# Performance work log

Hardware: AMD Instinct MI355X
Metric: run time of the kernel (lower is better)

The kernel has to match this reference:

```python
import jax, jax.numpy as jnp
import numpy as np

B, S, D = 2, 2048, 2048
H = 16
HD = D // H            # 128 head dim
L = 512                # latent dim
R = 64                 # rope dim (min(64, HD) = 64)
RH = R // 2
SCALE = HD ** -0.5     # note: uses head_dim, not head_dim+rope_dim
NEG = jnp.float32(-1e9)


def _rope_tables():
    inv_freq = 1.0 / (10000.0 ** (jnp.arange(0, R, 2, dtype=jnp.float32) / R))  # [RH]
    pos = jnp.arange(S, dtype=jnp.float32)
    freqs = pos[:, None] * inv_freq[None, :]  # [S, RH]
    return jnp.cos(freqs), jnp.sin(freqs)


def _apply_rope(x, cos, sin):
    # x: [B, H, S, R], interleaved even/odd rotation as in the torch source
    xe, xo = x[..., 0::2], x[..., 1::2]                    # [B,H,S,RH]
    c = cos[None, None]
    s = sin[None, None]
    re = xe * c - xo * s
    ro = xe * s + xo * c
    return jnp.stack([re, ro], axis=-1).reshape(x.shape)   # re-interleave


def setup_inputs() -> dict:
    key = jax.random.key(0)
    ks = jax.random.split(key, 8)
    std = 0.02
    f32 = jnp.float32
    return {
        "x":     jax.random.normal(ks[0], (B, S, D), f32),
        "W_ckv": jax.random.normal(ks[1], (D, L), f32) * std,      # compress_kv
        "W_kv":  jax.random.normal(ks[2], (L, 2 * D), f32) * std,  # kv_proj
        "W_cq":  jax.random.normal(ks[3], (D, L), f32) * std,      # compress_q
        "W_q":   jax.random.normal(ks[4], (L, D), f32) * std,      # q_proj
        "W_qr":  jax.random.normal(ks[5], (L, H * R), f32) * std,  # q_rope
        "W_kr":  jax.random.normal(ks[6], (L, R), f32) * std,      # k_rope
        "W_out": jax.random.normal(ks[7], (D, D), f32) * std,      # out_proj
    }


def reference(x, W_ckv, W_kv, W_cq, W_q, W_qr, W_kr, W_out):
    cos, sin = _rope_tables()

    c_kv = x @ W_ckv                                   # [B,S,L]
    kv = c_kv @ W_kv                                   # [B,S,2D]
    c_q = x @ W_cq                                     # [B,S,L]

    q_c = (c_q @ W_q).reshape(B, S, H, HD).transpose(0, 2, 1, 3)    # [B,H,S,HD]
    q_r = (c_q @ W_qr).reshape(B, S, H, R).transpose(0, 2, 1, 3)    # [B,H,S,R]
    k_r = (c_kv @ W_kr)[:, None, :, :]                               # [B,1,S,R]

    k_c, v = jnp.split(kv, 2, axis=-1)
    k_c = k_c.reshape(B, S, H, HD).transpose(0, 2, 1, 3)             # [B,H,S,HD]
    v = v.reshape(B, S, H, HD).transpose(0, 2, 1, 3)                 # [B,H,S,HD]

    q_r = _apply_rope(q_r, cos, sin)
    k_r = jnp.broadcast_to(_apply_rope(k_r, cos, sin), (B, H, S, R))

    q = jnp.concatenate([q_c, q_r], axis=-1)                         # [B,H,S,HD+R]
    k = jnp.concatenate([k_c, k_r], axis=-1)                         # [B,H,S,HD+R]

    scores = jnp.einsum("bhqd,bhkd->bhqk", q, k) * SCALE             # [B,H,S,S]
    causal = jnp.tril(jnp.ones((S, S), dtype=bool))
    scores = jnp.where(causal[None, None], scores, NEG)
    p = jax.nn.softmax(scores, axis=-1)
    attended = jnp.einsum("bhqk,bhkd->bhqd", p, v)                   # [B,H,S,HD]

    out = attended.transpose(0, 2, 1, 3).reshape(B, S, D) @ W_out    # [B,S,D]
    return out  # dropout is identity in eval / p=0
```

## Files before the change

### kernel.cpp

```cpp
#include <hip/hip_runtime.h>
#include <hip/hip_bf16.h>
#include <cstdint>
#include <cstddef>

typedef __bf16 bf16;
typedef __attribute__((ext_vector_type(2))) __bf16 bf16x2;
typedef __attribute__((ext_vector_type(4))) __bf16 bf16x4;
typedef __attribute__((ext_vector_type(8))) __bf16 bf16x8;
typedef __attribute__((ext_vector_type(4))) float f32x4;

#define MFMA16(a, b, c) __builtin_amdgcn_mfma_f32_16x16x32_bf16((a), (b), (c), 0, 0, 0)
#define SCALE_L2E 0.127517432f

#define QCR_STRIDE 3072
#define KV_STRIDE  4160

__device__ __forceinline__ void gload16(const void* g, void* l) {
    __builtin_amdgcn_global_load_lds(
        (const __attribute__((address_space(1))) void*)g,
        (__attribute__((address_space(3))) void*)l, 16, 0, 0);
}

__device__ __forceinline__ void bar_lgkm() {
    asm volatile("s_waitcnt lgkmcnt(0)" ::: "memory");
    __builtin_amdgcn_s_barrier();
    asm volatile("" ::: "memory");
}

__global__ void k_cvt(const float* __restrict__ in, bf16* __restrict__ out, int n4)
{
    int i = blockIdx.x * blockDim.x + threadIdx.x;
    int stride = gridDim.x * blockDim.x;
    const float4* in4 = (const float4*)in;
    bf16x4* o4 = (bf16x4*)out;
    for (; i < n4; i += stride) {
        float4 v = in4[i];
        bf16x4 o;
        o[0] = (bf16)v.x; o[1] = (bf16)v.y; o[2] = (bf16)v.z; o[3] = (bf16)v.w;
        o4[i] = o;
    }
}

__global__ __launch_bounds__(256) void k_cvtT(const float* __restrict__ in,
                                              bf16* __restrict__ out, int Kd, int Nd)
{
    __shared__ float tile[32][33];
    const int k0 = blockIdx.y * 32, n0 = blockIdx.x * 32;
    const int t = threadIdx.x;
    const int r = t >> 3, c4 = (t & 7) * 4;
    float4 v = *(const float4*)(in + (size_t)(k0 + r) * Nd + n0 + c4);
    tile[r][c4 + 0] = v.x; tile[r][c4 + 1] = v.y;
    tile[r][c4 + 2] = v.z; tile[r][c4 + 3] = v.w;
    __syncthreads();
    bf16x4 o;
    o[0] = (bf16)tile[c4 + 0][r]; o[1] = (bf16)tile[c4 + 1][r];
    o[2] = (bf16)tile[c4 + 2][r]; o[3] = (bf16)tile[c4 + 3][r];
    *(bf16x4*)(out + (size_t)(n0 + r) * Kd + k0 + c4) = o;
}

template<int NF, bool F32OUT>
__global__ __launch_bounds__(256) void k_gemm_bt(
    const bf16* __restrict__ A, const bf16* __restrict__ BT,
    bf16* __restrict__ Cb, float* __restrict__ Cf,
    int M, int N, int K, int lda)
{
    __shared__ bf16 As[2][4096];
    __shared__ bf16 Bs[2][NF * 1024];

    const int t = threadIdx.x;
    const int m0 = blockIdx.y * 128;
    const int n0 = blockIdx.x * (NF * 32);
    const int wid = t >> 6, lane = t & 63;
    const int wm = (wid >> 1) * 64, wn = (wid & 1) * (NF * 16);
    const int lr = lane & 15, lk = (lane >> 4) * 8;

    const int srow = t >> 2, skc = (t & 3) << 3;
    const int bn0 = min(n0 + srow, N - 1);
    const int bn1 = min(n0 + srow + 64, N - 1);

    f32x4 acc[4][NF];
    const f32x4 z = {0.f, 0.f, 0.f, 0.f};
#pragma unroll
    for (int m = 0; m < 4; ++m)
#pragma unroll
        for (int n = 0; n < NF; ++n) acc[m][n] = z;

    auto stage = [&](int buf, int k0) {
        gload16(BT + (size_t)bn0 * K + k0 + skc, &Bs[buf][t * 8]);
        if constexpr (NF == 4)
            gload16(BT + (size_t)bn1 * K + k0 + skc, &Bs[buf][(t + 256) * 8]);
        gload16(A + (size_t)(m0 + srow) * lda + k0 + skc, &As[buf][t * 8]);
        gload16(A + (size_t)(m0 + srow + 64) * lda + k0 + skc, &As[buf][(t + 256) * 8]);
    };

    stage(0, 0);
    __syncthreads();

    for (int k0 = 0; k0 < K; k0 += 32) {
        const int cur = (k0 >> 5) & 1;
        if (k0 + 32 < K) stage(cur ^ 1, k0 + 32);

        bf16x8 af[4], bfr[NF];
#pragma unroll
        for (int m = 0; m < 4; ++m) af[m] = *(const bf16x8*)(&As[cur][(wm + m * 16 + lr) * 32 + lk]);
#pragma unroll
        for (int n = 0; n < NF; ++n) bfr[n] = *(const bf16x8*)(&Bs[cur][(wn + n * 16 + lr) * 32 + lk]);
#pragma unroll
        for (int m = 0; m < 4; ++m)
#pragma unroll
            for (int n = 0; n < NF; ++n)
                acc[m][n] = MFMA16(af[m], bfr[n], acc[m][n]);

        __syncthreads();
    }

    const int lrow4 = (lane >> 4) * 4;
#pragma unroll
    for (int m = 0; m < 4; ++m)
#pragma unroll
        for (int n = 0; n < NF; ++n)
#pragma unroll
            for (int i = 0; i < 4; ++i) {
                int r = m0 + wm + m * 16 + lrow4 + i;
                int c = n0 + wn + n * 16 + lr;
                if (r < M && c < N) {
                    if constexpr (F32OUT) Cf[(size_t)r * N + c] = acc[m][n][i];
                    else Cb[(size_t)r * N + c] = (bf16)acc[m][n][i];
                }
            }
}

__global__ void k_rope_q(bf16* __restrict__ qcr)
{
    int idx = blockIdx.x * blockDim.x + threadIdx.x;
    int row = idx >> 9;
    int rem = idx & 511;
    int h = rem >> 5;
    int i = rem & 31;
    int s = row & 2047;
    float ang = (float)s * __expf(-(float)i * 0.28782313662f);
    float c = cosf(ang), sn = sinf(ang);
    size_t base = (size_t)row * QCR_STRIDE + 2048 + h * 64 + (i << 1);
    float xe = (float)qcr[base], xo = (float)qcr[base + 1];
    qcr[base] = (bf16)(xe * c - xo * sn);
    qcr[base + 1] = (bf16)(xe * sn + xo * c);
}

__global__ void k_rope_k(bf16* __restrict__ kvkr)
{
    int idx = blockIdx.x * blockDim.x + threadIdx.x;
    int row = idx >> 5;
    int i = idx & 31;
    int s = row & 2047;
    float ang = (float)s * __expf(-(float)i * 0.28782313662f);
    float c = cosf(ang), sn = sinf(ang);
    size_t base = (size_t)row * KV_STRIDE + 4096 + (i << 1);
    float xe = (float)kvkr[base], xo = (float)kvkr[base + 1];
    kvkr[base] = (bf16)(xe * c - xo * sn);
    kvkr[base + 1] = (bf16)(xe * sn + xo * c);
}

__global__ __launch_bounds__(512, 2) void k_attn(
    const bf16* __restrict__ qcr, const bf16* __restrict__ kvkr,
    bf16* __restrict__ att)
{
    __shared__ bf16 Ks[128 * 200];
    __shared__ bf16 Vt[128 * 136];
    __shared__ bf16 Pw[8][16 * 136];

    const int L = blockIdx.x;
    const int p = L >> 5;
    const int bh = L & 31;
    const int h = bh & 15, b = bh >> 4;

    const int t = threadIdx.x;
    const int wid = t >> 6, lane = t & 63;
    const int lr = lane & 15, lk = (lane >> 4) * 8, lrow4 = (lane >> 4) * 4;
    const size_t rowbase = (size_t)b * 2048;

    const int kcrow = t >> 4, kcfc = (t & 15) << 3;
    const int krrow = t >> 3, krfc = (t & 7) << 3;
    const int vk = (t & 63) * 2;
    const int vf = (t >> 6) * 8;

    const f32x4 z = {0.f, 0.f, 0.f, 0.f};

    bf16x8 rc[4], rr[2], rv[4];
    auto LOAD = [&](int kb) {
#pragma unroll
        for (int i = 0; i < 4; ++i)
            rc[i] = *(const bf16x8*)(kvkr + (rowbase + kb + kcrow + 32 * i) * KV_STRIDE + h * 128 + kcfc);
#pragma unroll
        for (int i = 0; i < 2; ++i)
            rr[i] = *(const bf16x8*)(kvkr + (rowbase + kb + krrow + 64 * i) * KV_STRIDE + 4096 + krfc);
#pragma unroll
        for (int i = 0; i < 2; ++i) {
            const bf16* vs = kvkr + (rowbase + kb + vk) * KV_STRIDE + 2048 + h * 128 + vf + 64 * i;
            rv[2 * i]     = *(const bf16x8*)vs;
            rv[2 * i + 1] = *(const bf16x8*)(vs + KV_STRIDE);
        }
    };
    auto WRITE = [&]() {
#pragma unroll
        for (int i = 0; i < 4; ++i)
            *(bf16x8*)(Ks + (kcrow + 32 * i) * 200 + kcfc) = rc[i];
#pragma unroll
        for (int i = 0; i < 2; ++i)
            *(bf16x8*)(Ks + (krrow + 64 * i) * 200 + 128 + krfc) = rr[i];
#pragma unroll
        for (int i = 0; i < 2; ++i)
#pragma unroll
            for (int j = 0; j < 8; ++j) {
                bf16x2 pr; pr[0] = rv[2 * i][j]; pr[1] = rv[2 * i + 1][j];
                *(bf16x2*)(Vt + (vf + 64 * i + j) * 136 + vk) = pr;
            }
    };

    LOAD(0);

#pragma unroll 1
    for (int pass = 0; pass < 2; ++pass) {
        const int qt = pass ? 15 - p : p;
        const int qrow_w = qt * 128 + wid * 16;

        bf16x8 qf[6];
        {
            const size_t qrow = rowbase + qrow_w + lr;
            const bf16* qp = qcr + qrow * QCR_STRIDE + h * 128;
#pragma unroll
            for (int ks = 0; ks < 4; ++ks) qf[ks] = *(const bf16x8*)(qp + ks * 32 + lk);
            const bf16* qp2 = qcr + qrow * QCR_STRIDE + 2048 + h * 64;
#pragma unroll
            for (int ks = 0; ks < 2; ++ks) qf[4 + ks] = *(const bf16x8*)(qp2 + ks * 32 + lk);
        }

        float mrow[4], lsum[4];
        f32x4 o[8];
#pragma unroll
        for (int i = 0; i < 4; ++i) { mrow[i] = -3e38f; lsum[i] = 0.f; }
#pragma unroll
        for (int n = 0; n < 8; ++n) o[n] = z;

        const int nkt = qt + 1;
#pragma unroll 1
        for (int kt = 0; kt < nkt; ++kt) {
            const int kb = kt * 128;
            bar_lgkm();
            WRITE();
            if (kt + 1 < nkt) LOAD(kb + 128);
            else if (pass == 0) LOAD(0);
            bar_lgkm();

            f32x4 sacc[8];
#pragma unroll
            for (int kg = 0; kg < 8; ++kg) {
                f32x4 s = z;
#pragma unroll
                for (int ks = 0; ks < 6; ++ks) {
                    bf16x8 kf = *(const bf16x8*)(Ks + (kg * 16 + lr) * 200 + ks * 32 + lk);
                    s = MFMA16(qf[ks], kf, s);
                }
                sacc[kg] = s;
            }

            const bool domask = (kb + 127) > qrow_w;
            float rmax[4];
#pragma unroll
            for (int i = 0; i < 4; ++i) {
                int qi = qrow_w + lrow4 + i;
                float mx = -3e38f;
#pragma unroll
                for (int kg = 0; kg < 8; ++kg) {
                    float v = sacc[kg][i] * SCALE_L2E;
                    if (domask && (kb + kg * 16 + lr) > qi) v = -3e38f;
                    sacc[kg][i] = v;
                    mx = fmaxf(mx, v);
                }
                rmax[i] = mx;
            }
#pragma unroll
            for (int d = 1; d < 16; d <<= 1)
#pragma unroll
                for (int i = 0; i < 4; ++i)
                    rmax[i] = fmaxf(rmax[i], __shfl_xor(rmax[i], d, 64));

            int anynew = 0;
#pragma unroll
            for (int i = 0; i < 4; ++i)
                if (rmax[i] > mrow[i]) anynew = 1;
            if (__any(anynew)) {
#pragma unroll
                for (int i = 0; i < 4; ++i) {
                    float mnew = fmaxf(mrow[i], rmax[i]);
                    float scl = __builtin_amdgcn_exp2f(mrow[i] - mnew);
                    mrow[i] = mnew;
                    lsum[i] *= scl;
#pragma unroll
                    for (int n = 0; n < 8; ++n) o[n][i] *= scl;
                }
            }

            float rsum[4] = {0.f, 0.f, 0.f, 0.f};
#pragma unroll
            for (int kg = 0; kg < 8; ++kg)
#pragma unroll
                for (int i = 0; i < 4; ++i) {
                    float pv = __builtin_amdgcn_exp2f(sacc[kg][i] - mrow[i]);
                    sacc[kg][i] = pv;
                    rsum[i] += pv;
                }
#pragma unroll
            for (int d = 1; d < 16; d <<= 1)
#pragma unroll
                for (int i = 0; i < 4; ++i) rsum[i] += __shfl_xor(rsum[i], d, 64);
#pragma unroll
            for (int i = 0; i < 4; ++i) lsum[i] += rsum[i];

#pragma unroll
            for (int kg = 0; kg < 8; ++kg)
#pragma unroll
                for (int i = 0; i < 4; ++i)
                    Pw[wid][(lrow4 + i) * 136 + kg * 16 + lr] = (bf16)sacc[kg][i];

#pragma unroll
            for (int ks = 0; ks < 4; ++ks) {
                bf16x8 pa = *(const bf16x8*)(&Pw[wid][lr * 136 + ks * 32 + lk]);
#pragma unroll
                for (int n = 0; n < 8; ++n) {
                    bf16x8 vfr = *(const bf16x8*)(Vt + (n * 16 + lr) * 136 + ks * 32 + lk);
                    o[n] = MFMA16(pa, vfr, o[n]);
                }
            }
        }

#pragma unroll
        for (int i = 0; i < 4; ++i) {
            float inv = 1.f / lsum[i];
            size_t orow = (rowbase + qrow_w + lrow4 + i) * 2048 + h * 128;
#pragma unroll
            for (int n = 0; n < 8; ++n)
                att[orow + n * 16 + lr] = (bf16)(o[n][i] * inv);
        }
    }
}

extern "C" void kernel_launch(void* const* d_in, const int* in_sizes, int n_in,
                              void* d_out, int out_size, void* d_ws, size_t ws_size,
                              hipStream_t stream)
{
    (void)in_sizes; (void)n_in; (void)out_size; (void)ws_size;
    const float* x = (const float*)d_in[0];
    const float* w_ckv = (const float*)d_in[1];
    const float* w_kv = (const float*)d_in[2];
    const float* w_cq = (const float*)d_in[3];
    const float* w_q = (const float*)d_in[4];
    const float* w_qr = (const float*)d_in[5];
    const float* w_kr = (const float*)d_in[6];
    const float* w_out = (const float*)d_in[7];
    float* out = (float*)d_out;

    char* ws = (char*)d_ws;
    size_t off = 0;
    auto take = [&](size_t elems) -> bf16* {
        bf16* p = (bf16*)(ws + off);
        off += (elems * sizeof(bf16) + 255) & ~(size_t)255;
        return p;
    };
    bf16* WCT    = take(1024ull * 2048);
    bf16* WKVKRT = take(4160ull * 512);
    bf16* WQQRT  = take(3072ull * 512);
    bf16* C      = take(4096ull * 1024);
    bf16* KVKR   = take(4096ull * 4160);
    bf16* QCR    = take(4096ull * 3072);
    bf16* ATT    = take(4096ull * 2048);
    bf16* WOUTT  = C;
    bf16* XB     = KVKR;

    auto cvtT = [&](const float* in, bf16* o, int K, int N) {
        k_cvtT<<<dim3(N / 32, K / 32), 256, 0, stream>>>(in, o, K, N);
    };
    cvtT(w_ckv, WCT, 2048, 512);
    cvtT(w_cq, WCT + 512ull * 2048, 2048, 512);
    cvtT(w_kv, WKVKRT, 512, 4096);
    cvtT(w_kr, WKVKRT + 4096ull * 512, 512, 64);
    cvtT(w_q, WQQRT, 512, 2048);
    cvtT(w_qr, WQQRT + 2048ull * 512, 512, 1024);

    k_cvt<<<2048, 256, 0, stream>>>(x, XB, (4096 * 2048) / 4);

    k_gemm_bt<2, false><<<dim3(16, 32), 256, 0, stream>>>(
        XB, WCT, C, nullptr, 4096, 1024, 2048, 2048);
    k_gemm_bt<4, false><<<dim3(33, 32), 256, 0, stream>>>(
        C, WKVKRT, KVKR, nullptr, 4096, 4160, 512, 1024);
    k_gemm_bt<4, false><<<dim3(24, 32), 256, 0, stream>>>(
        C + 512, WQQRT, QCR, nullptr, 4096, 3072, 512, 1024);

    cvtT(w_out, WOUTT, 2048, 2048);

    k_rope_q<<<8192, 256, 0, stream>>>(QCR);
    k_rope_k<<<512, 256, 0, stream>>>(KVKR);

    k_attn<<<256, 512, 0, stream>>>(QCR, KVKR, ATT);

    k_gemm_bt<4, true><<<dim3(16, 32), 256, 0, stream>>>(
        ATT, WOUTT, nullptr, out, 4096, 2048, 2048, 2048);
}
```

Measured before the change: 292.4 us.

## Split attention into one q-tile per block with 64-key tiles and folded scale

The attention kernel changes from 256 blocks that each process two paired q-tiles to 512 blocks with one q-tile each. Key tiles shrink from 128 to 64, which cuts LDS use so four blocks can be resident per CU. Warps skip key tiles that lie fully above their causal rows. The softmax scale times log2(e) is folded into the Q projection GEMM epilogue, and the row sums are taken with an extra MFMA against a ones vector instead of shuffle reductions. The cost is twice as many loop iterations and barriers per key, and the load balance now depends on block scheduling rather than explicit pairing.

```diff
diff --git a/kernel.cpp b/kernel.cpp
--- a/kernel.cpp
+++ b/kernel.cpp
@@ -62,7 +62,7 @@
 __global__ __launch_bounds__(256) void k_gemm_bt(
     const bf16* __restrict__ A, const bf16* __restrict__ BT,
     bf16* __restrict__ Cb, float* __restrict__ Cf,
-    int M, int N, int K, int lda)
+    int M, int N, int K, int lda, float cscale)
 {
     __shared__ bf16 As[2][4096];
     __shared__ bf16 Bs[2][NF * 1024];
@@ -124,8 +124,9 @@
                 int r = m0 + wm + m * 16 + lrow4 + i;
                 int c = n0 + wn + n * 16 + lr;
                 if (r < M && c < N) {
-                    if constexpr (F32OUT) Cf[(size_t)r * N + c] = acc[m][n][i];
-                    else Cb[(size_t)r * N + c] = (bf16)acc[m][n][i];
+                    float val = acc[m][n][i] * cscale;
+                    if constexpr (F32OUT) Cf[(size_t)r * N + c] = val;
+                    else Cb[(size_t)r * N + c] = (bf16)val;
                 }
             }
 }
@@ -160,17 +161,19 @@
     kvkr[base + 1] = (bf16)(xe * sn + xo * c);
 }
 
-__global__ __launch_bounds__(512, 2) void k_attn(
+__global__ __launch_bounds__(512, 4) void k_attn(
     const bf16* __restrict__ qcr, const bf16* __restrict__ kvkr,
     bf16* __restrict__ att)
 {
-    __shared__ bf16 Ks[128 * 200];
-    __shared__ bf16 Vt[128 * 136];
-    __shared__ bf16 Pw[8][16 * 136];
+    __shared__ bf16 Ks[64 * 200];
+    __shared__ bf16 Vt[128 * 72];
+    __shared__ bf16 Pw[8][16 * 72];
 
     const int L = blockIdx.x;
-    const int p = L >> 5;
-    const int bh = L & 31;
+    const int base = L & 255;
+    const int bh = base & 31;
+    const int qtg = base >> 5;
+    const int qt = (L < 256) ? qtg : 15 - qtg;
     const int h = bh & 15, b = bh >> 4;
 
     const int t = threadIdx.x;
@@ -180,167 +183,151 @@
 
     const int kcrow = t >> 4, kcfc = (t & 15) << 3;
     const int krrow = t >> 3, krfc = (t & 7) << 3;
-    const int vk = (t & 63) * 2;
-    const int vf = (t >> 6) * 8;
+    const int vk = (t & 31) * 2;
+    const int vf = (t >> 5) * 8;
 
     const f32x4 z = {0.f, 0.f, 0.f, 0.f};
 
-    bf16x8 rc[4], rr[2], rv[4];
+    bf16x8 rc0, rc1, rr, rv0, rv1;
     auto LOAD = [&](int kb) {
+        rc0 = *(const bf16x8*)(kvkr + (rowbase + kb + kcrow) * KV_STRIDE + h * 128 + kcfc);
+        rc1 = *(const bf16x8*)(kvkr + (rowbase + kb + kcrow + 32) * KV_STRIDE + h * 128 + kcfc);
+        rr  = *(const bf16x8*)(kvkr + (rowbase + kb + krrow) * KV_STRIDE + 4096 + krfc);
+        const bf16* vs = kvkr + (rowbase + kb + vk) * KV_STRIDE + 2048 + h * 128 + vf;
+        rv0 = *(const bf16x8*)vs;
+        rv1 = *(const bf16x8*)(vs + KV_STRIDE);
+    };
+    auto WRITE = [&]() {
+        *(bf16x8*)(Ks + kcrow * 200 + kcfc) = rc0;
+        *(bf16x8*)(Ks + (kcrow + 32) * 200 + kcfc) = rc1;
+        *(bf16x8*)(Ks + krrow * 200 + 128 + krfc) = rr;
+#pragma unroll
+        for (int j = 0; j < 8; ++j) {
+            bf16x2 pr; pr[0] = rv0[j]; pr[1] = rv1[j];
+            *(bf16x2*)(Vt + (vf + j) * 72 + vk) = pr;
+        }
+    };
+
+    const int qrow_w = qt * 128 + wid * 16;
+
+    bf16x8 qf[6];
+    {
+        const size_t qrow = rowbase + qrow_w + lr;
+        const bf16* qp = qcr + qrow * QCR_STRIDE + h * 128;
+#pragma unroll
+        for (int ks = 0; ks < 4; ++ks) qf[ks] = *(const bf16x8*)(qp + ks * 32 + lk);
+        const bf16* qp2 = qcr + qrow * QCR_STRIDE + 2048 + h * 64;
+#pragma unroll
+        for (int ks = 0; ks < 2; ++ks) qf[4 + ks] = *(const bf16x8*)(qp2 + ks * 32 + lk);
+    }
+
+    bf16x8 ones;
+#pragma unroll
+    for (int j = 0; j < 8; ++j) ones[j] = (bf16)1.0f;
+
+    float mrow[4], lsum[4];
+    f32x4 o[8];
+#pragma unroll
+    for (int i = 0; i < 4; ++i) { mrow[i] = -3e38f; lsum[i] = 0.f; }
+#pragma unroll
+    for (int n = 0; n < 8; ++n) o[n] = z;
+
+    const int nkt = 2 * qt + 2;
+    LOAD(0);
+
+#pragma unroll 1
+    for (int kt = 0; kt < nkt; ++kt) {
+        const int kb = kt * 64;
+        bar_lgkm();
+        WRITE();
+        if (kt + 1 < nkt) LOAD(kb + 64);
+        bar_lgkm();
+
+        if (kb > qrow_w + 15) continue;
+
+        f32x4 sacc[4];
+#pragma unroll
+        for (int kg = 0; kg < 4; ++kg) {
+            f32x4 s = z;
+#pragma unroll
+            for (int ks = 0; ks < 6; ++ks) {
+                bf16x8 kf = *(const bf16x8*)(Ks + (kg * 16 + lr) * 200 + ks * 32 + lk);
+                s = MFMA16(qf[ks], kf, s);
+            }
+            sacc[kg] = s;
+        }
+
+        const bool domask = (kb + 63) > qrow_w;
+        float rmax[4];
+#pragma unroll
+        for (int i = 0; i < 4; ++i) {
+            int qi = qrow_w + lrow4 + i;
+            float mx = -3e38f;
+#pragma unroll
+            for (int kg = 0; kg < 4; ++kg) {
+                float v = sacc[kg][i];
+                if (domask && (kb + kg * 16 + lr) > qi) v = -3e38f;
+                sacc[kg][i] = v;
+                mx = fmaxf(mx, v);
+            }
+            rmax[i] = mx;
+        }
+#pragma unroll
+        for (int d = 1; d < 16; d <<= 1)
+#pragma unroll
+            for (int i = 0; i < 4; ++i)
+                rmax[i] = fmaxf(rmax[i], __shfl_xor(rmax[i], d, 64));
+
+        int anynew = 0;
 #pragma unroll
         for (int i = 0; i < 4; ++i)
-            rc[i] = *(const bf16x8*)(kvkr + (rowbase + kb + kcrow + 32 * i) * KV_STRIDE + h * 128 + kcfc);
-#pragma unroll
-        for (int i = 0; i < 2; ++i)
-            rr[i] = *(const bf16x8*)(kvkr + (rowbase + kb + krrow + 64 * i) * KV_STRIDE + 4096 + krfc);
-#pragma unroll
-        for (int i = 0; i < 2; ++i) {
-            const bf16* vs = kvkr + (rowbase + kb + vk) * KV_STRIDE + 2048 + h * 128 + vf + 64 * i;
-            rv[2 * i]     = *(const bf16x8*)vs;
-            rv[2 * i + 1] = *(const bf16x8*)(vs + KV_STRIDE);
-        }
-    };
-    auto WRITE = [&]() {
-#pragma unroll
-        for (int i = 0; i < 4; ++i)
-            *(bf16x8*)(Ks + (kcrow + 32 * i) * 200 + kcfc) = rc[i];
-#pragma unroll
-        for (int i = 0; i < 2; ++i)
-            *(bf16x8*)(Ks + (krrow + 64 * i) * 200 + 128 + krfc) = rr[i];
-#pragma unroll
-        for (int i = 0; i < 2; ++i)
-#pragma unroll
-            for (int j = 0; j < 8; ++j) {
-                bf16x2 pr; pr[0] = rv[2 * i][j]; pr[1] = rv[2 * i + 1][j];
-                *(bf16x2*)(Vt + (vf + 64 * i + j) * 136 + vk) = pr;
-            }
-    };
-
-    LOAD(0);
-
-#pragma unroll 1
-    for (int pass = 0; pass < 2; ++pass) {
-        const int qt = pass ? 15 - p : p;
-        const int qrow_w = qt * 128 + wid * 16;
-
-        bf16x8 qf[6];
-        {
-            const size_t qrow = rowbase + qrow_w + lr;
-            const bf16* qp = qcr + qrow * QCR_STRIDE + h * 128;
-#pragma unroll
-            for (int ks = 0; ks < 4; ++ks) qf[ks] = *(const bf16x8*)(qp + ks * 32 + lk);
-            const bf16* qp2 = qcr + qrow * QCR_STRIDE + 2048 + h * 64;
-#pragma unroll
-            for (int ks = 0; ks < 2; ++ks) qf[4 + ks] = *(const bf16x8*)(qp2 + ks * 32 + lk);
-        }
-
-        float mrow[4], lsum[4];
-        f32x4 o[8];
-#pragma unroll
-        for (int i = 0; i < 4; ++i) { mrow[i] = -3e38f; lsum[i] = 0.f; }
-#pragma unroll
-        for (int n = 0; n < 8; ++n) o[n] = z;
-
-        const int nkt = qt + 1;
-#pragma unroll 1
-        for (int kt = 0; kt < nkt; ++kt) {
-            const int kb = kt * 128;
-            bar_lgkm();
-            WRITE();
-            if (kt + 1 < nkt) LOAD(kb + 128);
-            else if (pass == 0) LOAD(0);
-            bar_lgkm();
-
-            f32x4 sacc[8];
-#pragma unroll
-            for (int kg = 0; kg < 8; ++kg) {
-                f32x4 s = z;
-#pragma unroll
-                for (int ks = 0; ks < 6; ++ks) {
-                    bf16x8 kf = *(const bf16x8*)(Ks + (kg * 16 + lr) * 200 + ks * 32 + lk);
-                    s = MFMA16(qf[ks], kf, s);
-                }
-                sacc[kg] = s;
-            }
-
-            const bool domask = (kb + 127) > qrow_w;
-            float rmax[4];
+            if (rmax[i] > mrow[i]) anynew = 1;
+        if (__any(anynew)) {
 #pragma unroll
             for (int i = 0; i < 4; ++i) {
-                int qi = qrow_w + lrow4 + i;
-                float mx = -3e38f;
-#pragma unroll
-                for (int kg = 0; kg < 8; ++kg) {
-                    float v = sacc[kg][i] * SCALE_L2E;
-                    if (domask && (kb + kg * 16 + lr) > qi) v = -3e38f;
-                    sacc[kg][i] = v;
-                    mx = fmaxf(mx, v);
-                }
-                rmax[i] = mx;
-            }
-#pragma unroll
-            for (int d = 1; d < 16; d <<= 1)
-#pragma unroll
-                for (int i = 0; i < 4; ++i)
-                    rmax[i] = fmaxf(rmax[i], __shfl_xor(rmax[i], d, 64));
-
-            int anynew = 0;
+                float mnew = fmaxf(mrow[i], rmax[i]);
+                float scl = __builtin_amdgcn_exp2f(mrow[i] - mnew);
+                mrow[i] = mnew;
+                lsum[i] *= scl;
+#pragma unroll
+                for (int n = 0; n < 8; ++n) o[n][i] *= scl;
+            }
+        }
+
+#pragma unroll
+        for (int kg = 0; kg < 4; ++kg)
 #pragma unroll
             for (int i = 0; i < 4; ++i)
-                if (rmax[i] > mrow[i]) anynew = 1;
-            if (__any(anynew)) {
-#pragma unroll
-                for (int i = 0; i < 4; ++i) {
-                    float mnew = fmaxf(mrow[i], rmax[i]);
-                    float scl = __builtin_amdgcn_exp2f(mrow[i] - mnew);
-                    mrow[i] = mnew;
-                    lsum[i] *= scl;
-#pragma unroll
-                    for (int n = 0; n < 8; ++n) o[n][i] *= scl;
-                }
-            }
-
-            float rsum[4] = {0.f, 0.f, 0.f, 0.f};
-#pragma unroll
-            for (int kg = 0; kg < 8; ++kg)
-#pragma unroll
-                for (int i = 0; i < 4; ++i) {
-                    float pv = __builtin_amdgcn_exp2f(sacc[kg][i] - mrow[i]);
-                    sacc[kg][i] = pv;
-                    rsum[i] += pv;
-                }
-#pragma unroll
-            for (int d = 1; d < 16; d <<= 1)
-#pragma unroll
-                for (int i = 0; i < 4; ++i) rsum[i] += __shfl_xor(rsum[i], d, 64);
-#pragma unroll
-            for (int i = 0; i < 4; ++i) lsum[i] += rsum[i];
-
-#pragma unroll
-            for (int kg = 0; kg < 8; ++kg)
-#pragma unroll
-                for (int i = 0; i < 4; ++i)
-                    Pw[wid][(lrow4 + i) * 136 + kg * 16 + lr] = (bf16)sacc[kg][i];
-
-#pragma unroll
-            for (int ks = 0; ks < 4; ++ks) {
-                bf16x8 pa = *(const bf16x8*)(&Pw[wid][lr * 136 + ks * 32 + lk]);
-#pragma unroll
-                for (int n = 0; n < 8; ++n) {
-                    bf16x8 vfr = *(const bf16x8*)(Vt + (n * 16 + lr) * 136 + ks * 32 + lk);
-                    o[n] = MFMA16(pa, vfr, o[n]);
-                }
-            }
-        }
-
-#pragma unroll
-        for (int i = 0; i < 4; ++i) {
-            float inv = 1.f / lsum[i];
-            size_t orow = (rowbase + qrow_w + lrow4 + i) * 2048 + h * 128;
-#pragma unroll
-            for (int n = 0; n < 8; ++n)
-                att[orow + n * 16 + lr] = (bf16)(o[n][i] * inv);
-        }
+                sacc[kg][i] = __builtin_amdgcn_exp2f(sacc[kg][i] - mrow[i]);
+
+#pragma unroll
+        for (int kg = 0; kg < 4; ++kg)
+#pragma unroll
+            for (int i = 0; i < 4; ++i)
+                Pw[wid][(lrow4 + i) * 72 + kg * 16 + lr] = (bf16)sacc[kg][i];
+
+        f32x4 rs = z;
+#pragma unroll
+        for (int ks = 0; ks < 2; ++ks) {
+            bf16x8 pa = *(const bf16x8*)(&Pw[wid][lr * 72 + ks * 32 + lk]);
+            rs = MFMA16(pa, ones, rs);
+#pragma unroll
+            for (int n = 0; n < 8; ++n) {
+                bf16x8 vfr = *(const bf16x8*)(Vt + (n * 16 + lr) * 72 + ks * 32 + lk);
+                o[n] = MFMA16(pa, vfr, o[n]);
+            }
+        }
+#pragma unroll
+        for (int i = 0; i < 4; ++i) lsum[i] += rs[i];
+    }
+
+#pragma unroll
+    for (int i = 0; i < 4; ++i) {
+        float inv = 1.f / lsum[i];
+        size_t orow = (rowbase + qrow_w + lrow4 + i) * 2048 + h * 128;
+#pragma unroll
+        for (int n = 0; n < 8; ++n)
+            att[orow + n * 16 + lr] = (bf16)(o[n][i] * inv);
     }
 }
 
@@ -389,19 +376,19 @@
     k_cvt<<<2048, 256, 0, stream>>>(x, XB, (4096 * 2048) / 4);
 
     k_gemm_bt<2, false><<<dim3(16, 32), 256, 0, stream>>>(
-        XB, WCT, C, nullptr, 4096, 1024, 2048, 2048);
+        XB, WCT, C, nullptr, 4096, 1024, 2048, 2048, 1.0f);
     k_gemm_bt<4, false><<<dim3(33, 32), 256, 0, stream>>>(
-        C, WKVKRT, KVKR, nullptr, 4096, 4160, 512, 1024);
+        C, WKVKRT, KVKR, nullptr, 4096, 4160, 512, 1024, 1.0f);
     k_gemm_bt<4, false><<<dim3(24, 32), 256, 0, stream>>>(
-        C + 512, WQQRT, QCR, nullptr, 4096, 3072, 512, 1024);
+        C + 512, WQQRT, QCR, nullptr, 4096, 3072, 512, 1024, SCALE_L2E);
 
     cvtT(w_out, WOUTT, 2048, 2048);
 
     k_rope_q<<<8192, 256, 0, stream>>>(QCR);
     k_rope_k<<<512, 256, 0, stream>>>(KVKR);
 
-    k_attn<<<256, 512, 0, stream>>>(QCR, KVKR, ATT);
+    k_attn<<<512, 512, 0, stream>>>(QCR, KVKR, ATT);
 
     k_gemm_bt<4, true><<<dim3(16, 32), 256, 0, stream>>>(
-        ATT, WOUTT, nullptr, out, 4096, 2048, 2048, 2048);
-}
+        ATT, WOUTT, nullptr, out, 4096, 2048, 2048, 2048, 1.0f);
+}
```

New measurement: 304.3 us. 4.1% more time.
